# Performance work log

Measured on AMD Instinct MI355X. Metric: run time of the kernel, lower is better.

## Reference

```python
import jax, jax.numpy as jnp
import numpy as np

NUM_HEADS = 16
TOP_K = 6


def setup_inputs() -> dict:
    key = jax.random.key(0)
    ks = jax.random.split(key, 16)
    B, P = 8192, 4096
    QD = PD = D = 1024  # query_dim, prototype_dim, token_dim
    s = lambda d: 1.0 / np.sqrt(d)
    return {
        "query": jax.random.normal(ks[0], (B, QD), jnp.float32),
        "prototype_bank": jax.random.normal(ks[1], (P, PD), jnp.float32),
        "prototype_logits": jax.random.normal(ks[2], (B, P), jnp.float32),
        # query_proj / prototype_proj (torch Linear: y = x @ W.T + b)
        "Wq_proj": jax.random.normal(ks[3], (D, QD), jnp.float32) * s(QD),
        "bq_proj": jnp.zeros((D,), jnp.float32),
        "Wp_proj": jax.random.normal(ks[4], (D, PD), jnp.float32) * s(PD),
        "bp_proj": jnp.zeros((D,), jnp.float32),
        # MultiheadAttention in-proj (q, k, v) and out-proj
        "Wq": jax.random.normal(ks[5], (D, D), jnp.float32) * s(D),
        "bq": jnp.zeros((D,), jnp.float32),
        "Wk": jax.random.normal(ks[6], (D, D), jnp.float32) * s(D),
        "bk": jnp.zeros((D,), jnp.float32),
        "Wv": jax.random.normal(ks[7], (D, D), jnp.float32) * s(D),
        "bv": jnp.zeros((D,), jnp.float32),
        "Wo": jax.random.normal(ks[8], (D, D), jnp.float32) * s(D),
        "bo": jnp.zeros((D,), jnp.float32),
    }


def reference(query, prototype_bank, prototype_logits,
              Wq_proj, bq_proj, Wp_proj, bp_proj,
              Wq, bq, Wk, bk, Wv, bv, Wo, bo):
    B, D = query.shape[0], Wq.shape[0]
    h = NUM_HEADS
    dh = D // h
    k = min(TOP_K, prototype_bank.shape[0])

    # top-k prototype selection (indices only)
    _, topk_idx = jax.lax.top_k(prototype_logits, k)            # [B, k]

    projected_bank = prototype_bank @ Wp_proj.T + bp_proj        # [P, D]
    selected = projected_bank[topk_idx]                          # [B, k, D]

    attn_query = (query @ Wq_proj.T + bq_proj)[:, None, :]       # [B, 1, D]

    # MultiheadAttention (batch_first, eval mode so dropout is a no-op)
    qh = (attn_query @ Wq.T + bq).reshape(B, 1, h, dh).transpose(0, 2, 1, 3)  # [B,h,1,dh]
    kh = (selected @ Wk.T + bk).reshape(B, k, h, dh).transpose(0, 2, 1, 3)    # [B,h,k,dh]
    vh = (selected @ Wv.T + bv).reshape(B, k, h, dh).transpose(0, 2, 1, 3)    # [B,h,k,dh]

    scores = jnp.einsum("bhqd,bhkd->bhqk", qh, kh) / jnp.sqrt(jnp.float32(dh))
    w = jax.nn.softmax(scores, axis=-1)                          # [B,h,1,k]
    ctx = jnp.einsum("bhqk,bhkd->bhqd", w, vh)                   # [B,h,1,dh]
    ctx = ctx.transpose(0, 2, 1, 3).reshape(B, 1, D)
    context = ctx @ Wo.T + bo                                    # [B,1,D]

    attn_weights = w.mean(axis=1)                                # avg heads -> [B,1,k]
    return context[:, 0, :], attn_weights[:, 0, :]
```

## Files before the change

kernel.cpp:

```cpp
#include <hip/hip_runtime.h>
#include <stdint.h>

#define B_ROWS 8192
#define P_ROWS 4096
#define D_DIM  1024
#define K_TOP  6

typedef __attribute__((ext_vector_type(8))) short short8;
typedef __attribute__((ext_vector_type(4))) float floatx4;

static __device__ __forceinline__ float bf2f(unsigned short h) {
  return __uint_as_float(((unsigned)h) << 16);
}
static __device__ __forceinline__ unsigned short f2bf(float f) {
  unsigned u = __float_as_uint(f);
  u += 0x7FFFu + ((u >> 16) & 1u);
  return (unsigned short)(u >> 16);
}

typedef __attribute__((address_space(3))) unsigned int lds32_t;
typedef const __attribute__((address_space(1))) unsigned int g32_t;

static __device__ __forceinline__ void gld_lds16(const unsigned short* g, unsigned short* l) {
  __builtin_amdgcn_global_load_lds((g32_t*)(uintptr_t)g,
                                   (lds32_t*)(unsigned int)(uintptr_t)l, 16, 0, 0);
}

template <bool OUT_BF16, bool HAS_BIAS>
static __device__ __forceinline__ void gemm_bt_body(
    const unsigned short* __restrict__ A, const unsigned short* __restrict__ Bw,
    const float* __restrict__ bias, void* __restrict__ Cout, int m0, int n0) {
  constexpr int Kd = 1024, Nd = 1024, BK = 64;
  __shared__ unsigned short sA[128 * BK];
  __shared__ unsigned short sB[128 * BK];

  const int tid = threadIdx.x;
  const int wid = tid >> 6, lane = tid & 63;
  const int wm = (wid & 1) * 64, wn = (wid >> 1) * 64;

  floatx4 acc[4][4];
#pragma unroll
  for (int mt = 0; mt < 4; ++mt)
#pragma unroll
    for (int nt = 0; nt < 4; ++nt) acc[mt][nt] = (floatx4){0.f, 0.f, 0.f, 0.f};

  const int ld_row = lane >> 3;
  const int ld_col = (lane & 7) * 8;

  for (int kt = 0; kt < Kd / BK; ++kt) {
    const int k0 = kt * BK;
    __syncthreads();
#pragma unroll
    for (int c = 0; c < 4; ++c) {
      const int ch = wid * 4 + c;
      const int r = ch * 8 + ld_row;
      gld_lds16(A  + (size_t)(m0 + r) * Kd + k0 + ld_col, sA + ch * 512);
      gld_lds16(Bw + (size_t)(n0 + r) * Kd + k0 + ld_col, sB + ch * 512);
    }
    __syncthreads();
#pragma unroll
    for (int ks = 0; ks < 2; ++ks) {
      const int kk = ks * 32 + (lane >> 4) * 8;
      short8 a[4], b[4];
#pragma unroll
      for (int t = 0; t < 4; ++t) {
        a[t] = *(const short8*)(sA + (wm + t * 16 + (lane & 15)) * BK + kk);
        b[t] = *(const short8*)(sB + (wn + t * 16 + (lane & 15)) * BK + kk);
      }
#pragma unroll
      for (int mt = 0; mt < 4; ++mt)
#pragma unroll
        for (int nt = 0; nt < 4; ++nt)
          acc[mt][nt] = __builtin_amdgcn_mfma_f32_16x16x32_bf16(a[mt], b[nt], acc[mt][nt], 0, 0, 0);
    }
  }

  const int er = lane >> 4;
  const int ec = lane & 15;
#pragma unroll
  for (int mt = 0; mt < 4; ++mt) {
#pragma unroll
    for (int nt = 0; nt < 4; ++nt) {
      const int col = n0 + wn + nt * 16 + ec;
      const float bv = HAS_BIAS ? bias[col] : 0.f;
#pragma unroll
      for (int r = 0; r < 4; ++r) {
        const int row = m0 + wm + mt * 16 + er * 4 + r;
        const float v = acc[mt][nt][r] + bv;
        if (OUT_BF16)
          ((unsigned short*)Cout)[(size_t)row * Nd + col] = f2bf(v);
        else
          ((float*)Cout)[(size_t)row * Nd + col] = v;
      }
    }
  }
}

template <bool OUT_BF16>
__global__ __launch_bounds__(256) void gemm_bt_kernel(
    const unsigned short* __restrict__ A, const unsigned short* __restrict__ Bw,
    const float* __restrict__ bias, void* __restrict__ Cout) {
  gemm_bt_body<OUT_BF16, true>(A, Bw, bias, Cout, blockIdx.y * 128, blockIdx.x * 128);
}

static __device__ __forceinline__ void cswap64(unsigned long long& hi, unsigned long long& lo) {
  unsigned long long x = hi, y = lo;
  bool c = y > x;
  hi = c ? y : x;
  lo = c ? x : y;
}

static __device__ __forceinline__ unsigned long long topk_key(float val, int idx) {
  unsigned u = __float_as_uint(val);
  u ^= ((unsigned)((int)u >> 31)) | 0x80000000u;
  return (((unsigned long long)u) << 32) | (unsigned long long)(0xFFFFFFFFu - (unsigned)idx);
}

#define PREP_BLOCKS 19712
struct PrepArgs {
  const float* cs[6]; unsigned short* cd[6];
  const float* ts[2]; unsigned short* td[2];
  const float* bW[3]; const float* bp[3]; const float* bb[3]; float* bo[3];
  const float* logits; int* topk;
};

__global__ __launch_bounds__(256) void prep_kernel(PrepArgs a) {
  const int b0 = blockIdx.x;
  if (b0 < 2048) {
    __shared__ int s_cnt[4];
    __shared__ unsigned long long s_cand[4][64];
    const int wid = threadIdx.x >> 6;
    const int lane = threadIdx.x & 63;
    const int row = b0 * 4 + wid;
    const float4* lp4 = (const float4*)(a.logits + (size_t)row * P_ROWS);

    float4 r[16];
#pragma unroll
    for (int j = 0; j < 16; ++j) r[j] = lp4[j * 64 + lane];
    float mx = -1e38f;
#pragma unroll
    for (int j = 0; j < 16; ++j)
      mx = fmaxf(mx, fmaxf(fmaxf(r[j].x, r[j].y), fmaxf(r[j].z, r[j].w)));

    float mkeep = mx, tau = mx;
#pragma unroll
    for (int it = 0; it < K_TOP; ++it) {
      float best = mkeep;
#pragma unroll
      for (int o = 32; o > 0; o >>= 1) best = fmaxf(best, __shfl_xor(best, o));
      tau = best;
      if (it < K_TOP - 1) mkeep = (mkeep == best) ? -1e38f : mkeep;
    }

    if (lane == 0) s_cnt[wid] = 0;

#pragma unroll
    for (int j = 0; j < 16; ++j) {
      const int base = j * 256 + lane * 4;
      const float4 v = r[j];
      if (v.x >= tau) { int s = atomicAdd(&s_cnt[wid], 1); if (s < 64) s_cand[wid][s] = topk_key(v.x, base); }
      if (v.y >= tau) { int s = atomicAdd(&s_cnt[wid], 1); if (s < 64) s_cand[wid][s] = topk_key(v.y, base + 1); }
      if (v.z >= tau) { int s = atomicAdd(&s_cnt[wid], 1); if (s < 64) s_cand[wid][s] = topk_key(v.z, base + 2); }
      if (v.w >= tau) { int s = atomicAdd(&s_cnt[wid], 1); if (s < 64) s_cand[wid][s] = topk_key(v.w, base + 3); }
    }
    const int n = s_cnt[wid];

    if (n <= 64) {
      unsigned long long key = (lane < n) ? s_cand[wid][lane] : 0ull;
#pragma unroll
      for (int it = 0; it < K_TOP; ++it) {
        unsigned long long best = key;
#pragma unroll
        for (int o = 32; o > 0; o >>= 1) {
          unsigned long long t = __shfl_xor(best, o);
          best = t > best ? t : best;
        }
        if (lane == 0)
          a.topk[row * K_TOP + it] = (int)(0xFFFFFFFFu - (unsigned)(best & 0xFFFFFFFFull));
        key = (key == best) ? 0ull : key;
      }
    } else {
      unsigned long long m0 = 0, m1 = 0, m2 = 0, m3 = 0, m4 = 0, m5 = 0;
      auto ins = [&](float val, int idx) {
        unsigned long long key = topk_key(val, idx);
        m5 = key > m5 ? key : m5;
        cswap64(m4, m5);
        cswap64(m3, m4);
        cswap64(m2, m3);
        cswap64(m1, m2);
        cswap64(m0, m1);
      };
#pragma unroll
      for (int j = 0; j < 16; ++j) {
        const int base = j * 256 + lane * 4;
        ins(r[j].x, base);
        ins(r[j].y, base + 1);
        ins(r[j].z, base + 2);
        ins(r[j].w, base + 3);
      }
#pragma unroll
      for (int it = 0; it < K_TOP; ++it) {
        unsigned long long best = m0;
#pragma unroll
        for (int o = 32; o > 0; o >>= 1) {
          unsigned long long t = __shfl_xor(best, o);
          best = t > best ? t : best;
        }
        if (lane == 0)
          a.topk[row * K_TOP + it] = (int)(0xFFFFFFFFu - (unsigned)(best & 0xFFFFFFFFull));
        const bool pred = (m0 == best);
        m0 = pred ? m1 : m0;
        m1 = pred ? m2 : m1;
        m2 = pred ? m3 : m2;
        m3 = pred ? m4 : m3;
        m4 = pred ? m5 : m4;
        m5 = pred ? 0ull : m5;
      }
    }
    return;
  }
  const int b = b0 - 2048;
  if (b < 16384) {
    int seg; unsigned sb;
    if (b < 8192) { seg = 0; sb = 0; }
    else if (b < 12288) { seg = 1; sb = 8192; }
    else { seg = 2 + ((b - 12288) >> 10); sb = 12288u + (((unsigned)(seg - 2)) << 10); }
    const unsigned off = (((unsigned)b - sb) << 10) + threadIdx.x * 4u;
    float4 v = *(const float4*)(a.cs[seg] + off);
    ushort4 o;
    o.x = f2bf(v.x); o.y = f2bf(v.y); o.z = f2bf(v.z); o.w = f2bf(v.w);
    *(ushort4*)(a.cd[seg] + off) = o;
  } else if (b < 16896) {
    __shared__ unsigned short t[64][72];
    const int tt = b - 16384;
    const int which = tt >> 8;
    const int tile = tt & 255;
    const int i0 = (tile >> 4) * 64, j0 = (tile & 15) * 64;
    const float* src = a.ts[which];
    unsigned short* dst = a.td[which];
    const int r = threadIdx.x >> 4;
    const int c = (threadIdx.x & 15) * 4;
#pragma unroll
    for (int rr = 0; rr < 4; ++rr) {
      const int row = r + rr * 16;
      float4 v = *(const float4*)(src + (size_t)(i0 + row) * D_DIM + j0 + c);
      t[c + 0][row] = f2bf(v.x); t[c + 1][row] = f2bf(v.y);
      t[c + 2][row] = f2bf(v.z); t[c + 3][row] = f2bf(v.w);
    }
    __syncthreads();
#pragma unroll
    for (int rr = 0; rr < 4; ++rr) {
      const int row = r + rr * 16;
      ushort4 v = *(const ushort4*)(&t[row][c]);
      *(ushort4*)(dst + (size_t)(j0 + row) * D_DIM + i0 + c) = v;
    }
  } else {
    const int b3 = b - 16896;
    const int j = b3 >> 8;
    const int nb = b3 & 255;
    const int wid = threadIdx.x >> 6, lane = threadIdx.x & 63;
    const int n = nb * 4 + wid;
    const float* W = a.bW[j] + (size_t)n * D_DIM;
    const float* p = a.bp[j];
    float s = 0.f;
#pragma unroll
    for (int d = lane; d < D_DIM; d += 64) s += W[d] * p[d];
#pragma unroll
    for (int o = 32; o > 0; o >>= 1) s += __shfl_xor(s, o);
    if (lane == 0) a.bo[j][n] = s + a.bb[j][n];
  }
}

#define MID_BLOCKS 192
struct MidArgs {
  const unsigned short* fA[3]; const unsigned short* fW[3]; unsigned short* fC[3];
};

__global__ __launch_bounds__(256) void mid_kernel(MidArgs a) {
  const int z = blockIdx.x >> 6;
  const int tile = blockIdx.x & 63;
  gemm_bt_body<true, false>(a.fA[z], a.fW[z], nullptr, (void*)a.fC[z],
                            (tile >> 3) * 128, (tile & 7) * 128);
}

#define GEMM3_BLOCKS 1024
struct Gemm3Args {
  const unsigned short* A[3]; const unsigned short* W[3]; const float* bias[3];
  unsigned short* C[3];
};

__global__ __launch_bounds__(256) void gemm3_kernel(Gemm3Args a) {
  const int b = blockIdx.x;
  int seg, lb;
  if (b < 512) { seg = 0; lb = b; }
  else if (b < 768) { seg = 1; lb = b - 512; }
  else { seg = 2; lb = b - 768; }
  gemm_bt_body<true, true>(a.A[seg], a.W[seg], a.bias[seg], (void*)a.C[seg],
                           (lb >> 3) * 128, (lb & 7) * 128);
}

__global__ __launch_bounds__(256) void attn_kernel(
    const unsigned short* __restrict__ q2,
    const unsigned short* __restrict__ kb,
    const unsigned short* __restrict__ vb,
    const int* __restrict__ topk,
    unsigned short* __restrict__ ctx,
    float* __restrict__ attnw) {
  const int b = blockIdx.x;
  const int wid = threadIdx.x >> 6, lane = threadIdx.x & 63;
  __shared__ float wsum[4][K_TOP];

  int idx[K_TOP];
#pragma unroll
  for (int j = 0; j < K_TOP; ++j) idx[j] = topk[b * K_TOP + j];

  float hw[K_TOP] = {0.f, 0.f, 0.f, 0.f, 0.f, 0.f};
#pragma unroll
  for (int hh = 0; hh < 4; ++hh) {
    const int h = wid * 4 + hh;
    const int off = h * 64 + lane;
    const float qv = bf2f(q2[(size_t)b * D_DIM + off]);
    float s[K_TOP];
#pragma unroll
    for (int j = 0; j < K_TOP; ++j)
      s[j] = qv * bf2f(kb[(size_t)idx[j] * D_DIM + off]);
#pragma unroll
    for (int j = 0; j < K_TOP; ++j)
#pragma unroll
      for (int o = 32; o > 0; o >>= 1) s[j] += __shfl_xor(s[j], o);

    float mx = -1e30f;
#pragma unroll
    for (int j = 0; j < K_TOP; ++j) mx = fmaxf(mx, s[j] * 0.125f);
    float e[K_TOP], sum = 0.f;
#pragma unroll
    for (int j = 0; j < K_TOP; ++j) { e[j] = __expf(s[j] * 0.125f - mx); sum += e[j]; }
    const float inv = 1.0f / sum;

    float o = 0.f;
#pragma unroll
    for (int j = 0; j < K_TOP; ++j) {
      const float w = e[j] * inv;
      hw[j] += w;
      o += w * bf2f(vb[(size_t)idx[j] * D_DIM + off]);
    }
    ctx[(size_t)b * D_DIM + off] = f2bf(o);
  }
  if (lane == 0) {
#pragma unroll
    for (int j = 0; j < K_TOP; ++j) wsum[wid][j] = hw[j];
  }
  __syncthreads();
  if (threadIdx.x < K_TOP) {
    const float t = wsum[0][threadIdx.x] + wsum[1][threadIdx.x] +
                    wsum[2][threadIdx.x] + wsum[3][threadIdx.x];
    attnw[(size_t)b * K_TOP + threadIdx.x] = t * (1.0f / 16.0f);
  }
}

extern "C" void kernel_launch(void* const* d_in, const int* in_sizes, int n_in,
                              void* d_out, int out_size, void* d_ws, size_t ws_size,
                              hipStream_t stream) {
  const float* query   = (const float*)d_in[0];
  const float* bank    = (const float*)d_in[1];
  const float* logits  = (const float*)d_in[2];
  const float* Wq_proj = (const float*)d_in[3];
  const float* bq_proj = (const float*)d_in[4];
  const float* Wp_proj = (const float*)d_in[5];
  const float* bp_proj = (const float*)d_in[6];
  const float* Wq      = (const float*)d_in[7];
  const float* bq      = (const float*)d_in[8];
  const float* Wk      = (const float*)d_in[9];
  const float* bk      = (const float*)d_in[10];
  const float* Wv      = (const float*)d_in[11];
  const float* bv      = (const float*)d_in[12];
  const float* Wo      = (const float*)d_in[13];
  const float* bo      = (const float*)d_in[14];

  char* ws = (char*)d_ws;
  size_t off = 0;
  auto alloc = [&](size_t bytes) {
    void* p = ws + off;
    off += (bytes + 255) & ~(size_t)255;
    return p;
  };
  unsigned short* q_bf    = (unsigned short*)alloc((size_t)B_ROWS * D_DIM * 2);
  unsigned short* bank_bf = (unsigned short*)alloc((size_t)P_ROWS * D_DIM * 2);
  unsigned short* q2_bf   = (unsigned short*)alloc((size_t)B_ROWS * D_DIM * 2);
  unsigned short* kb_bf   = (unsigned short*)alloc((size_t)P_ROWS * D_DIM * 2);
  unsigned short* vb_bf   = (unsigned short*)alloc((size_t)P_ROWS * D_DIM * 2);
  unsigned short* wq_bf   = (unsigned short*)alloc((size_t)D_DIM * D_DIM * 2);
  unsigned short* wk_bf   = (unsigned short*)alloc((size_t)D_DIM * D_DIM * 2);
  unsigned short* wv_bf   = (unsigned short*)alloc((size_t)D_DIM * D_DIM * 2);
  unsigned short* wo_bf   = (unsigned short*)alloc((size_t)D_DIM * D_DIM * 2);
  unsigned short* wqpT_bf = (unsigned short*)alloc((size_t)D_DIM * D_DIM * 2);
  unsigned short* wppT_bf = (unsigned short*)alloc((size_t)D_DIM * D_DIM * 2);
  unsigned short* wcq_bf  = (unsigned short*)alloc((size_t)D_DIM * D_DIM * 2);
  unsigned short* wck_bf  = (unsigned short*)alloc((size_t)D_DIM * D_DIM * 2);
  unsigned short* wcv_bf  = (unsigned short*)alloc((size_t)D_DIM * D_DIM * 2);
  float* bcq              = (float*)alloc(D_DIM * 4);
  float* bck              = (float*)alloc(D_DIM * 4);
  float* bcv              = (float*)alloc(D_DIM * 4);
  int* topk               = (int*)alloc((size_t)B_ROWS * K_TOP * 4);

  float* out_ctx  = (float*)d_out;
  float* out_attn = out_ctx + (size_t)B_ROWS * D_DIM;
  (void)out_ctx;

  PrepArgs pa;
  pa.cs[0] = query; pa.cd[0] = q_bf;
  pa.cs[1] = bank;  pa.cd[1] = bank_bf;
  pa.cs[2] = Wq;    pa.cd[2] = wq_bf;
  pa.cs[3] = Wk;    pa.cd[3] = wk_bf;
  pa.cs[4] = Wv;    pa.cd[4] = wv_bf;
  pa.cs[5] = Wo;    pa.cd[5] = wo_bf;
  pa.ts[0] = Wq_proj; pa.td[0] = wqpT_bf;
  pa.ts[1] = Wp_proj; pa.td[1] = wppT_bf;
  pa.bW[0] = Wq; pa.bp[0] = bq_proj; pa.bb[0] = bq; pa.bo[0] = bcq;
  pa.bW[1] = Wk; pa.bp[1] = bp_proj; pa.bb[1] = bk; pa.bo[1] = bck;
  pa.bW[2] = Wv; pa.bp[2] = bp_proj; pa.bb[2] = bv; pa.bo[2] = bcv;
  pa.logits = logits; pa.topk = topk;
  prep_kernel<<<PREP_BLOCKS, 256, 0, stream>>>(pa);

  MidArgs ma;
  ma.fA[0] = wq_bf; ma.fW[0] = wqpT_bf; ma.fC[0] = wcq_bf;
  ma.fA[1] = wk_bf; ma.fW[1] = wppT_bf; ma.fC[1] = wck_bf;
  ma.fA[2] = wv_bf; ma.fW[2] = wppT_bf; ma.fC[2] = wcv_bf;
  mid_kernel<<<MID_BLOCKS, 256, 0, stream>>>(ma);

  Gemm3Args ga;
  ga.A[0] = q_bf;    ga.W[0] = wcq_bf; ga.bias[0] = bcq; ga.C[0] = q2_bf;
  ga.A[1] = bank_bf; ga.W[1] = wck_bf; ga.bias[1] = bck; ga.C[1] = kb_bf;
  ga.A[2] = bank_bf; ga.W[2] = wcv_bf; ga.bias[2] = bcv; ga.C[2] = vb_bf;
  gemm3_kernel<<<GEMM3_BLOCKS, 256, 0, stream>>>(ga);

  attn_kernel<<<B_ROWS, 256, 0, stream>>>(q2_bf, kb_bf, vb_bf, topk, q_bf, out_attn);

  dim3 grid2(D_DIM / 128, B_ROWS / 128);
  gemm_bt_kernel<false><<<grid2, 256, 0, stream>>>(q_bf, wo_bf, bo, d_out);
}
```

Before: 436.7 us.

## Rebalance top-k to one row per block and attention to one row per wave

```diff
diff --git a/kernel.cpp b/kernel.cpp
--- a/kernel.cpp
+++ b/kernel.cpp
@@ -116,7 +116,7 @@
   return (((unsigned long long)u) << 32) | (unsigned long long)(0xFFFFFFFFu - (unsigned)idx);
 }
 
-#define PREP_BLOCKS 19712
+#define PREP_BLOCKS 25856
 struct PrepArgs {
   const float* cs[6]; unsigned short* cd[6];
   const float* ts[2]; unsigned short* td[2];
@@ -126,23 +126,28 @@
 
 __global__ __launch_bounds__(256) void prep_kernel(PrepArgs a) {
   const int b0 = blockIdx.x;
-  if (b0 < 2048) {
-    __shared__ int s_cnt[4];
-    __shared__ unsigned long long s_cand[4][64];
-    const int wid = threadIdx.x >> 6;
-    const int lane = threadIdx.x & 63;
-    const int row = b0 * 4 + wid;
+  if (b0 < 8192) {
+    __shared__ float s_tau[4];
+    __shared__ int s_cnt;
+    __shared__ unsigned long long s_cand[128];
+    const int row = b0;
+    const int tid = threadIdx.x;
+    const int wid = tid >> 6, lane = tid & 63;
     const float4* lp4 = (const float4*)(a.logits + (size_t)row * P_ROWS);
 
-    float4 r[16];
-#pragma unroll
-    for (int j = 0; j < 16; ++j) r[j] = lp4[j * 64 + lane];
-    float mx = -1e38f;
-#pragma unroll
-    for (int j = 0; j < 16; ++j)
-      mx = fmaxf(mx, fmaxf(fmaxf(r[j].x, r[j].y), fmaxf(r[j].z, r[j].w)));
-
-    float mkeep = mx, tau = mx;
+    float4 r0 = lp4[tid];
+    float4 r1 = lp4[256 + tid];
+    float4 r2 = lp4[512 + tid];
+    float4 r3 = lp4[768 + tid];
+    if (tid == 0) s_cnt = 0;
+
+    float tmax =
+        fmaxf(fmaxf(fmaxf(fmaxf(r0.x, r0.y), fmaxf(r0.z, r0.w)),
+                    fmaxf(fmaxf(r1.x, r1.y), fmaxf(r1.z, r1.w))),
+              fmaxf(fmaxf(fmaxf(r2.x, r2.y), fmaxf(r2.z, r2.w)),
+                    fmaxf(fmaxf(r3.x, r3.y), fmaxf(r3.z, r3.w))));
+
+    float mkeep = tmax, tau = tmax;
 #pragma unroll
     for (int it = 0; it < K_TOP; ++it) {
       float best = mkeep;
@@ -151,25 +156,31 @@
       tau = best;
       if (it < K_TOP - 1) mkeep = (mkeep == best) ? -1e38f : mkeep;
     }
-
-    if (lane == 0) s_cnt[wid] = 0;
-
-#pragma unroll
-    for (int j = 0; j < 16; ++j) {
-      const int base = j * 256 + lane * 4;
-      const float4 v = r[j];
-      if (v.x >= tau) { int s = atomicAdd(&s_cnt[wid], 1); if (s < 64) s_cand[wid][s] = topk_key(v.x, base); }
-      if (v.y >= tau) { int s = atomicAdd(&s_cnt[wid], 1); if (s < 64) s_cand[wid][s] = topk_key(v.y, base + 1); }
-      if (v.z >= tau) { int s = atomicAdd(&s_cnt[wid], 1); if (s < 64) s_cand[wid][s] = topk_key(v.z, base + 2); }
-      if (v.w >= tau) { int s = atomicAdd(&s_cnt[wid], 1); if (s < 64) s_cand[wid][s] = topk_key(v.w, base + 3); }
-    }
-    const int n = s_cnt[wid];
-
-    if (n <= 64) {
-      unsigned long long key = (lane < n) ? s_cand[wid][lane] : 0ull;
+    if (lane == 0) s_tau[wid] = tau;
+    __syncthreads();
+    tau = fmaxf(fmaxf(s_tau[0], s_tau[1]), fmaxf(s_tau[2], s_tau[3]));
+
+    auto push = [&](float v, int idx) {
+      if (v >= tau) {
+        int s = atomicAdd(&s_cnt, 1);
+        if (s < 128) s_cand[s] = topk_key(v, idx);
+      }
+    };
+    const int e0 = tid * 4, e1 = 1024 + tid * 4, e2 = 2048 + tid * 4, e3 = 3072 + tid * 4;
+    push(r0.x, e0); push(r0.y, e0 + 1); push(r0.z, e0 + 2); push(r0.w, e0 + 3);
+    push(r1.x, e1); push(r1.y, e1 + 1); push(r1.z, e1 + 2); push(r1.w, e1 + 3);
+    push(r2.x, e2); push(r2.y, e2 + 1); push(r2.z, e2 + 2); push(r2.w, e2 + 3);
+    push(r3.x, e3); push(r3.y, e3 + 1); push(r3.z, e3 + 2); push(r3.w, e3 + 3);
+    __syncthreads();
+    const int n = s_cnt;
+    if (wid != 0) return;
+
+    if (n <= 128) {
+      unsigned long long k0 = (lane < n) ? s_cand[lane] : 0ull;
+      unsigned long long k1 = (lane + 64 < n) ? s_cand[lane + 64] : 0ull;
 #pragma unroll
       for (int it = 0; it < K_TOP; ++it) {
-        unsigned long long best = key;
+        unsigned long long best = k0 > k1 ? k0 : k1;
 #pragma unroll
         for (int o = 32; o > 0; o >>= 1) {
           unsigned long long t = __shfl_xor(best, o);
@@ -177,7 +188,8 @@
         }
         if (lane == 0)
           a.topk[row * K_TOP + it] = (int)(0xFFFFFFFFu - (unsigned)(best & 0xFFFFFFFFull));
-        key = (key == best) ? 0ull : key;
+        k0 = (k0 == best) ? 0ull : k0;
+        k1 = (k1 == best) ? 0ull : k1;
       }
     } else {
       unsigned long long m0 = 0, m1 = 0, m2 = 0, m3 = 0, m4 = 0, m5 = 0;
@@ -190,13 +202,13 @@
         cswap64(m1, m2);
         cswap64(m0, m1);
       };
-#pragma unroll
       for (int j = 0; j < 16; ++j) {
+        float4 v = lp4[j * 64 + lane];
         const int base = j * 256 + lane * 4;
-        ins(r[j].x, base);
-        ins(r[j].y, base + 1);
-        ins(r[j].z, base + 2);
-        ins(r[j].w, base + 3);
+        ins(v.x, base);
+        ins(v.y, base + 1);
+        ins(v.z, base + 2);
+        ins(v.w, base + 3);
       }
 #pragma unroll
       for (int it = 0; it < K_TOP; ++it) {
@@ -219,7 +231,7 @@
     }
     return;
   }
-  const int b = b0 - 2048;
+  const int b = b0 - 8192;
   if (b < 16384) {
     int seg; unsigned sb;
     if (b < 8192) { seg = 0; sb = 0; }
@@ -306,55 +318,94 @@
     const int* __restrict__ topk,
     unsigned short* __restrict__ ctx,
     float* __restrict__ attnw) {
-  const int b = blockIdx.x;
   const int wid = threadIdx.x >> 6, lane = threadIdx.x & 63;
-  __shared__ float wsum[4][K_TOP];
+  const int b = blockIdx.x * 4 + wid;
 
   int idx[K_TOP];
 #pragma unroll
   for (int j = 0; j < K_TOP; ++j) idx[j] = topk[b * K_TOP + j];
 
-  float hw[K_TOP] = {0.f, 0.f, 0.f, 0.f, 0.f, 0.f};
-#pragma unroll
-  for (int hh = 0; hh < 4; ++hh) {
-    const int h = wid * 4 + hh;
-    const int off = h * 64 + lane;
-    const float qv = bf2f(q2[(size_t)b * D_DIM + off]);
-    float s[K_TOP];
+  const short8* q2r = (const short8*)(q2 + (size_t)b * D_DIM);
+  short8 qv0 = q2r[lane], qv1 = q2r[64 + lane];
+  float q0[8], q1[8];
+#pragma unroll
+  for (int i = 0; i < 8; ++i) {
+    q0[i] = bf2f((unsigned short)qv0[i]);
+    q1[i] = bf2f((unsigned short)qv1[i]);
+  }
+
+  float s0[K_TOP], s1[K_TOP];
+#pragma unroll
+  for (int j = 0; j < K_TOP; ++j) {
+    const short8* kr = (const short8*)(kb + (size_t)idx[j] * D_DIM);
+    short8 k0 = kr[lane], k1 = kr[64 + lane];
+    float p0 = 0.f, p1 = 0.f;
+#pragma unroll
+    for (int i = 0; i < 8; ++i) {
+      p0 += q0[i] * bf2f((unsigned short)k0[i]);
+      p1 += q1[i] * bf2f((unsigned short)k1[i]);
+    }
+    s0[j] = p0; s1[j] = p1;
+  }
+#pragma unroll
+  for (int j = 0; j < K_TOP; ++j) {
+#pragma unroll
+    for (int o = 1; o < 8; o <<= 1) {
+      s0[j] += __shfl_xor(s0[j], o);
+      s1[j] += __shfl_xor(s1[j], o);
+    }
+  }
+
+  float mx0 = -1e30f, mx1 = -1e30f;
+#pragma unroll
+  for (int j = 0; j < K_TOP; ++j) {
+    mx0 = fmaxf(mx0, s0[j] * 0.125f);
+    mx1 = fmaxf(mx1, s1[j] * 0.125f);
+  }
+  float w0[K_TOP], w1[K_TOP], sum0 = 0.f, sum1 = 0.f;
+#pragma unroll
+  for (int j = 0; j < K_TOP; ++j) {
+    w0[j] = __expf(s0[j] * 0.125f - mx0); sum0 += w0[j];
+    w1[j] = __expf(s1[j] * 0.125f - mx1); sum1 += w1[j];
+  }
+  const float inv0 = 1.0f / sum0, inv1 = 1.0f / sum1;
+#pragma unroll
+  for (int j = 0; j < K_TOP; ++j) { w0[j] *= inv0; w1[j] *= inv1; }
+
+  float o0[8], o1[8];
+#pragma unroll
+  for (int i = 0; i < 8; ++i) { o0[i] = 0.f; o1[i] = 0.f; }
+#pragma unroll
+  for (int j = 0; j < K_TOP; ++j) {
+    const short8* vr = (const short8*)(vb + (size_t)idx[j] * D_DIM);
+    short8 v0 = vr[lane], v1 = vr[64 + lane];
+#pragma unroll
+    for (int i = 0; i < 8; ++i) {
+      o0[i] += w0[j] * bf2f((unsigned short)v0[i]);
+      o1[i] += w1[j] * bf2f((unsigned short)v1[i]);
+    }
+  }
+  short8 c0, c1;
+#pragma unroll
+  for (int i = 0; i < 8; ++i) {
+    c0[i] = (short)f2bf(o0[i]);
+    c1[i] = (short)f2bf(o1[i]);
+  }
+  short8* cr = (short8*)(ctx + (size_t)b * D_DIM);
+  cr[lane] = c0;
+  cr[64 + lane] = c1;
+
+  float t[K_TOP];
+#pragma unroll
+  for (int j = 0; j < K_TOP; ++j) t[j] = w0[j] + w1[j];
+#pragma unroll
+  for (int j = 0; j < K_TOP; ++j)
+#pragma unroll
+    for (int o = 32; o > 0; o >>= 1) t[j] += __shfl_xor(t[j], o);
+  if (lane == 0) {
 #pragma unroll
     for (int j = 0; j < K_TOP; ++j)
-      s[j] = qv * bf2f(kb[(size_t)idx[j] * D_DIM + off]);
-#pragma unroll
-    for (int j = 0; j < K_TOP; ++j)
-#pragma unroll
-      for (int o = 32; o > 0; o >>= 1) s[j] += __shfl_xor(s[j], o);
-
-    float mx = -1e30f;
-#pragma unroll
-    for (int j = 0; j < K_TOP; ++j) mx = fmaxf(mx, s[j] * 0.125f);
-    float e[K_TOP], sum = 0.f;
-#pragma unroll
-    for (int j = 0; j < K_TOP; ++j) { e[j] = __expf(s[j] * 0.125f - mx); sum += e[j]; }
-    const float inv = 1.0f / sum;
-
-    float o = 0.f;
-#pragma unroll
-    for (int j = 0; j < K_TOP; ++j) {
-      const float w = e[j] * inv;
-      hw[j] += w;
-      o += w * bf2f(vb[(size_t)idx[j] * D_DIM + off]);
-    }
-    ctx[(size_t)b * D_DIM + off] = f2bf(o);
-  }
-  if (lane == 0) {
-#pragma unroll
-    for (int j = 0; j < K_TOP; ++j) wsum[wid][j] = hw[j];
-  }
-  __syncthreads();
-  if (threadIdx.x < K_TOP) {
-    const float t = wsum[0][threadIdx.x] + wsum[1][threadIdx.x] +
-                    wsum[2][threadIdx.x] + wsum[3][threadIdx.x];
-    attnw[(size_t)b * K_TOP + threadIdx.x] = t * (1.0f / 16.0f);
+      attnw[(size_t)b * K_TOP + j] = t[j] * (1.0f / 128.0f);
   }
 }
 
@@ -434,7 +485,7 @@
   ga.A[2] = bank_bf; ga.W[2] = wcv_bf; ga.bias[2] = bcv; ga.C[2] = vb_bf;
   gemm3_kernel<<<GEMM3_BLOCKS, 256, 0, stream>>>(ga);
 
-  attn_kernel<<<B_ROWS, 256, 0, stream>>>(q2_bf, kb_bf, vb_bf, topk, q_bf, out_attn);
+  attn_kernel<<<B_ROWS / 4, 256, 0, stream>>>(q2_bf, kb_bf, vb_bf, topk, q_bf, out_attn);
 
   dim3 grid2(D_DIM / 128, B_ROWS / 128);
   gemm_bt_kernel<false><<<grid2, 256, 0, stream>>>(q_bf, wo_bf, bo, d_out);
```

Result: faster. 407.2 us (-6.8%).
